# Optimization experiments

Measured on AMD Instinct MI355X. Metric: run time of the kernel, lower is better.

Reference implementation:

```python
import jax, jax.numpy as jnp
import numpy as np

LSTM_SIZE = 64
NUM_OPS = 5
NUM_LAYERS = 7  # 2 warmup anchors + 5 sampled layers (layer_id 2..6)


def _lstm_cell(x, h, c, w_ih, w_hh, b_ih, b_hh):
    # torch LSTMCell gate order: i, f, g, o
    g = x @ w_ih.T + b_ih + h @ w_hh.T + b_hh  # [1, 4*64]
    i, f, gg, o = jnp.split(g, 4, axis=1)
    c2 = jax.nn.sigmoid(f) * c + jax.nn.sigmoid(i) * jnp.tanh(gg)
    h2 = jax.nn.sigmoid(o) * jnp.tanh(c2)
    return h2, c2


def _sampler(embed, w_ih, w_hh, b_ih, b_hh, w_soft, b_soft, b_soft_no_learn,
             w_attn1, w_attn2, v_attn, prev_c, prev_h, use_bias, key):
    keys = jax.random.split(key, 20)  # 5 layers * (2 index + 2 op) samples
    k = 0
    anchors, anchors_w1, arc_seq = [], [], []
    log_prob = jnp.float32(0.0)
    entropy = jnp.float32(0.0)
    inputs = embed[0][None, :]
    # warmup: two anchor slots (anchors are zeros, per original code)
    for _ in range(2):
        prev_h, prev_c = _lstm_cell(inputs, prev_h, prev_c, w_ih, w_hh, b_ih, b_hh)
        anchors.append(jnp.zeros((1, LSTM_SIZE), jnp.float32))
        anchors_w1.append(prev_h @ w_attn1.T)
    for layer_id in range(2, NUM_LAYERS):
        idxs, ops = [], []
        # sample 2 previous-layer indices via tiny attention
        for _ in range(2):
            prev_h, prev_c = _lstm_cell(inputs, prev_h, prev_c, w_ih, w_hh, b_ih, b_hh)
            query = jnp.concatenate(anchors_w1, axis=0)            # [layer_id, 64]
            q = jnp.tanh(query + prev_h @ w_attn2.T)               # broadcast [layer_id, 64]
            logits = (q @ v_attn.T).reshape(layer_id)              # [layer_id]
            logits = logits / 5.0 + 1.1 * jnp.tanh(logits)
            index = jax.random.categorical(keys[k], logits); k += 1
            logp = jax.nn.log_softmax(logits)
            log_prob = log_prob + (-logp[index])
            entropy = entropy + jax.lax.stop_gradient(-jnp.sum(logp * jnp.exp(logp)))
            idxs.append(index)
            A = jnp.concatenate(anchors, axis=0)                   # [layer_id, 64]
            inputs = A[index][None, :]
        # sample 2 ops
        for _ in range(2):
            prev_h, prev_c = _lstm_cell(inputs, prev_h, prev_c, w_ih, w_hh, b_ih, b_hh)
            logits = (prev_h @ w_soft.T + b_soft)                  # [1, 5]
            logits = 1.1 / 2.5 * jnp.tanh(logits / 5.0)
            if use_bias:
                logits = logits + b_soft_no_learn
            logits = logits[0]
            op_id = jax.random.categorical(keys[k], logits); k += 1
            logp = jax.nn.log_softmax(logits)
            log_prob = log_prob + (-logp[op_id])
            entropy = entropy + jax.lax.stop_gradient(-jnp.sum(logp * jnp.exp(logp)))
            ops.append(op_id)
            inputs = embed[op_id + 1][None, :]
        # extra step producing this layer's anchor
        prev_h, prev_c = _lstm_cell(inputs, prev_h, prev_c, w_ih, w_hh, b_ih, b_hh)
        anchors.append(prev_h)
        anchors_w1.append(prev_h @ w_attn1.T)
        inputs = embed[0][None, :]
        # arc layout per layer after in-place fixups: [idx1, op1, idx2, op2]
        arc_seq += [idxs[0], ops[0], idxs[1], ops[1]]
    arc = jnp.stack(arc_seq)
    return arc, entropy, log_prob, prev_c, prev_h


def setup_inputs() -> dict:
    key = jax.random.key(0)
    ks = jax.random.split(key, 9)
    u = lambda k, shape: jax.random.uniform(k, shape, jnp.float32, -0.1, 0.1)
    return {
        "embed": u(ks[0], (6, LSTM_SIZE)),
        "w_ih": u(ks[1], (4 * LSTM_SIZE, LSTM_SIZE)),
        "w_hh": u(ks[2], (4 * LSTM_SIZE, LSTM_SIZE)),
        "b_ih": u(ks[3], (4 * LSTM_SIZE,)),
        "b_hh": u(ks[4], (4 * LSTM_SIZE,)),
        "w_soft": u(ks[5], (NUM_OPS, LSTM_SIZE)),
        "b_soft": jnp.array([[10.0, 10.0, 0.0, 0.0, 0.0]], jnp.float32),
        "b_soft_no_learn": jnp.array([[0.25, 0.25, -0.25, -0.25, -0.25]], jnp.float32),
        "w_attn1": u(ks[6], (LSTM_SIZE, LSTM_SIZE)),
        "w_attn2": u(ks[7], (LSTM_SIZE, LSTM_SIZE)),
        "v_attn": u(ks[8], (1, LSTM_SIZE)),
        "seed": 0,
    }


def reference(embed, w_ih, w_hh, b_ih, b_hh, w_soft, b_soft, b_soft_no_learn,
              w_attn1, w_attn2, v_attn, seed):
    key = jax.random.key(seed)
    k1, k2 = jax.random.split(key)
    zc = jnp.zeros((1, LSTM_SIZE), jnp.float32)
    zh = jnp.zeros((1, LSTM_SIZE), jnp.float32)
    arc1, ent1, lp1, c, h = _sampler(embed, w_ih, w_hh, b_ih, b_hh, w_soft, b_soft,
                                     b_soft_no_learn, w_attn1, w_attn2, v_attn,
                                     zc, zh, True, k1)
    arc2, ent2, lp2, _, _ = _sampler(embed, w_ih, w_hh, b_ih, b_hh, w_soft, b_soft,
                                     b_soft_no_learn, w_attn1, w_attn2, v_attn,
                                     c, h, False, k2)
    return (arc1, arc2, lp1 + lp2, ent1 + ent2)
```

## Files before the change

kernel.cpp:

```cpp
#include <hip/hip_runtime.h>
#include <cstdint>

#ifndef FASTMATH
#define FASTMATH 1
#endif

#define NT 512

__device__ __forceinline__ uint32_t rotl32_(uint32_t v, int d) {
  return (v << d) | (v >> (32 - d));
}

__device__ __forceinline__ void tf2x32(uint32_t k0, uint32_t k1,
                                       uint32_t x0, uint32_t x1,
                                       uint32_t& o0, uint32_t& o1) {
  const uint32_t k2 = k0 ^ k1 ^ 0x1BD11BDAu;
  x0 += k0; x1 += k1;
#define TF4(a,b,c,d) \
  x0 += x1; x1 = rotl32_(x1,a); x1 ^= x0; \
  x0 += x1; x1 = rotl32_(x1,b); x1 ^= x0; \
  x0 += x1; x1 = rotl32_(x1,c); x1 ^= x0; \
  x0 += x1; x1 = rotl32_(x1,d); x1 ^= x0;
  TF4(13,15,26,6)
  x0 += k1; x1 += k2 + 1u;
  TF4(17,29,16,24)
  x0 += k2; x1 += k0 + 2u;
  TF4(13,15,26,6)
  x0 += k0; x1 += k1 + 3u;
  TF4(17,29,16,24)
  x0 += k1; x1 += k2 + 4u;
  TF4(13,15,26,6)
  x0 += k2; x1 += k0 + 5u;
#undef TF4
  o0 = x0; o1 = x1;
}

#if FASTMATH
__device__ __forceinline__ float tanh_(float x) {
  float e = __expf(2.0f * x);
  return 1.0f - __fdividef(2.0f, e + 1.0f);
}
__device__ __forceinline__ float sig_(float x) {
  return __fdividef(1.0f, 1.0f + __expf(-x));
}
#define log_ __logf
#define exp_ __expf
#else
__device__ __forceinline__ float tanh_(float x) { return tanhf(x); }
__device__ __forceinline__ float sig_(float x) { return 0.5f * tanhf(0.5f * x) + 0.5f; }
#define log_ logf
#define exp_ expf
#endif

template <int CTRL>
__device__ __forceinline__ float dppf(float x) {
  return __int_as_float(__builtin_amdgcn_update_dpp(
      0, __float_as_int(x), CTRL, 0xF, 0xF, true));
}
template <int CTRL>
__device__ __forceinline__ int dppi(int x) {
  return __builtin_amdgcn_update_dpp(0, x, CTRL, 0xF, 0xF, true);
}
constexpr int QP1 = 0xB1;
constexpr int QP2 = 0x4E;
constexpr int HM  = 0x141;

__global__ __launch_bounds__(NT, 1)
void nas_controller(const float* __restrict__ embed,
                    const float* __restrict__ w_ih,
                    const float* __restrict__ w_hh,
                    const float* __restrict__ b_ih,
                    const float* __restrict__ b_hh,
                    const float* __restrict__ w_soft,
                    const float* __restrict__ b_soft,
                    const float* __restrict__ b_soft_nl,
                    const float* __restrict__ w_attn1,
                    const float* __restrict__ w_attn2,
                    const float* __restrict__ v_attn,
                    const int* __restrict__ seedp,
                    float* __restrict__ out) {
  const int tid  = threadIdx.x;
  const int lane = tid & 63;
  const int wid  = tid >> 6;
  const int row  = tid >> 1;
  const int half = tid & 1;

  __shared__ __align__(16) float attn1L[64 * 68];
  __shared__ __align__(16) float attn2L[64 * 68];
  __shared__ __align__(16) float wsoftL[5 * 68 + 8];
  __shared__ __align__(16) float vaL[64];
  __shared__ __align__(16) float preQ[13 * 256];
  __shared__ __align__(16) float aw1sL[8 * 68];
  __shared__ __align__(16) float hw2L[64];
  __shared__ __align__(16) float hB[64];
  __shared__ float gates[2][256];
  __shared__ float gL[320];
  __shared__ float lSave[320];
  __shared__ float lpT[40], entT[40];
  __shared__ int   biSave[40];
  __shared__ float bsoftL[8], bnlL[8];

  float4 wi[8], wh[8];
  {
    const float4* a = reinterpret_cast<const float4*>(w_ih) + row * 16 + half * 8;
#pragma unroll
    for (int j = 0; j < 8; ++j) wi[j] = a[j];
    const float4* b = reinterpret_cast<const float4*>(w_hh) + row * 16 + half * 8;
#pragma unroll
    for (int j = 0; j < 8; ++j) wh[j] = b[j];
  }
  const float bsi = b_ih[lane] + b_hh[lane];
  const float bsf = b_ih[64 + lane] + b_hh[64 + lane];
  const float bsg = b_ih[128 + lane] + b_hh[128 + lane];
  const float bso = b_ih[192 + lane] + b_hh[192 + lane];

  for (int i4 = tid; i4 < 1024; i4 += NT) {
    int r = i4 >> 4, c4 = i4 & 15;
    reinterpret_cast<float4*>(attn1L)[r * 17 + c4] =
        reinterpret_cast<const float4*>(w_attn1)[i4];
    reinterpret_cast<float4*>(attn2L)[r * 17 + c4] =
        reinterpret_cast<const float4*>(w_attn2)[i4];
  }
  for (int i = tid; i < 340; i += NT) {
    int r = i / 68, c = i % 68;
    wsoftL[i] = (c < 64) ? w_soft[r * 64 + c] : 0.f;
  }
  if (tid < 64) { vaL[tid] = v_attn[tid]; hB[tid] = 0.f; }
  if (tid < 256) gates[0][tid] = 0.f;
  if (tid < 8) {
    bsoftL[tid] = (tid < 5) ? b_soft[tid] : 0.f;
    bnlL[tid]   = (tid < 5) ? b_soft_nl[tid] : 0.f;
  }
  preQ[6 * 256 + tid] = 0.f;

  if (tid < 320) {
    int s_ = (tid >= 160) ? 1 : 0;
    int rem = tid - s_ * 160;
    int k = rem >> 3, i = rem & 7;
    uint32_t a, b, ka, kb, o0, o1;
    tf2x32(0u, (uint32_t)seedp[0], 0u, (uint32_t)s_, a, b);
    tf2x32(a, b, 0u, (uint32_t)k, ka, kb);
    tf2x32(ka, kb, 0u, (uint32_t)i, o0, o1);
    uint32_t bits = o0 ^ o1;
    const float TINY = 1.1754943508222875e-38f;
    float uu = __uint_as_float((bits >> 9) | 0x3f800000u) - 1.0f;
    uu = uu * (1.0f - TINY) + TINY;
    uu = fmaxf(TINY, uu);
    gL[tid] = -log_(-log_(uu));
  }

#pragma unroll
  for (int e = 0; e < 6; ++e) {
    const float4* x4 = reinterpret_cast<const float4*>(embed + e * 64) + half * 8;
    float a0 = 0, a1 = 0, a2 = 0, a3 = 0;
#pragma unroll
    for (int j = 0; j < 8; ++j) {
      float4 x = x4[j], w = wi[j];
      a0 = fmaf(w.x, x.x, a0); a1 = fmaf(w.y, x.y, a1);
      a2 = fmaf(w.z, x.z, a2); a3 = fmaf(w.w, x.w, a3);
    }
    float acc = (a0 + a1) + (a2 + a3);
    acc += __shfl_xor(acc, 1);
    if (half == 0) preQ[e * 256 + row] = acc;
  }

  __syncthreads();

  float creg = 0.f;
  int gp = 0, sIdx = 0;
  int srcSlot = 0;

  auto nonlinW0 = [&]() {
    const float* pq = preQ + srcSlot * 256;
    float gi = (gates[gp][lane]       + pq[lane])       + bsi;
    float gf = (gates[gp][64 + lane]  + pq[64 + lane])  + bsf;
    float gg = (gates[gp][128 + lane] + pq[128 + lane]) + bsg;
    float go = (gates[gp][192 + lane] + pq[192 + lane]) + bso;
    float c2 = sig_(gf) * creg + sig_(gi) * tanh_(gg);
    float h2 = sig_(go) * tanh_(c2);
    creg = c2;
    hB[lane] = h2;
  };

  auto hdotGW = [&]() {
    const float4* h4 = reinterpret_cast<const float4*>(hB) + half * 8;
    float a0 = 0, a1 = 0, a2 = 0, a3 = 0;
#pragma unroll
    for (int j = 0; j < 8; ++j) {
      float4 x = h4[j], w = wh[j];
      a0 = fmaf(w.x, x.x, a0); a1 = fmaf(w.y, x.y, a1);
      a2 = fmaf(w.z, x.z, a2); a3 = fmaf(w.w, x.w, a3);
    }
    float acc = (a0 + a1) + (a2 + a3);
    acc += __shfl_xor(acc, 1);
    if (half == 0) gates[gp ^ 1][row] = acc;
  };

  auto matvecAll = [&](const float* W, float* dst) {
    const int r8 = tid >> 3, q = tid & 7;
    const float4* w4 = reinterpret_cast<const float4*>(W + r8 * 68 + q * 8);
    float4 wa = w4[0], wb = w4[1];
    const float4* h4 = reinterpret_cast<const float4*>(hB) + q * 2;
    float4 ha = h4[0], hb = h4[1];
    float acc = fmaf(wa.x, ha.x, fmaf(wa.y, ha.y, fmaf(wa.z, ha.z, wa.w * ha.w)));
    acc += fmaf(wb.x, hb.x, fmaf(wb.y, hb.y, fmaf(wb.z, hb.z, wb.w * hb.w)));
    acc += __shfl_xor(acc, 1);
    acc += __shfl_xor(acc, 2);
    acc += __shfl_xor(acc, 4);
    if (q == 0) dst[r8] = acc;
  };

  auto anchorPre = [&](int slot) {
    const float4* h4 = reinterpret_cast<const float4*>(hB) + half * 8;
    float a0 = 0, a1 = 0, a2 = 0, a3 = 0;
#pragma unroll
    for (int j = 0; j < 8; ++j) {
      float4 x = h4[j], w = wi[j];
      a0 = fmaf(w.x, x.x, a0); a1 = fmaf(w.y, x.y, a1);
      a2 = fmaf(w.z, x.z, a2); a3 = fmaf(w.w, x.w, a3);
    }
    float acc = (a0 + a1) + (a2 + a3);
    acc += __shfl_xor(acc, 1);
    if (half == 0) preQ[slot * 256 + row] = acc;
  };

  auto argmaxSel = [&](int n, int k, float l, float* op) -> int {
    if (lane < 8) lSave[(sIdx * 20 + k) * 8 + lane] = l;
    float g = (lane < n) ? gL[sIdx * 160 + k * 8 + lane] : 0.f;
    float v = (lane < n) ? (l + g) : -INFINITY;
    int bi = lane & 7;
#define ARGSTEP(C) { float ov = dppf<C>(v); int oi = dppi<C>(bi); \
    bool tk = (ov > v) || (ov == v && oi < bi); if (tk) { v = ov; bi = oi; } }
    ARGSTEP(QP1) ARGSTEP(QP2) ARGSTEP(HM)
#undef ARGSTEP
    if (lane == 0) {
      biSave[sIdx * 20 + k] = bi;
      op[0] = (float)bi;
    }
    return __builtin_amdgcn_readfirstlane(bi);
  };

  auto idxSel = [&](int n, int k, float* op) -> int {
    const int g8 = lane >> 3, j = lane & 7;
    float sacc = 0.f;
    if (g8 < n) {
      const float4* aw = reinterpret_cast<const float4*>(aw1sL + g8 * 68 + j * 8);
      const float4* hq = reinterpret_cast<const float4*>(hw2L + j * 8);
      const float4* vq = reinterpret_cast<const float4*>(vaL + j * 8);
      float4 A0 = aw[0], A1 = aw[1], H0 = hq[0], H1 = hq[1], V0 = vq[0], V1 = vq[1];
      sacc = fmaf(tanh_(A0.x + H0.x), V0.x, sacc);
      sacc = fmaf(tanh_(A0.y + H0.y), V0.y, sacc);
      sacc = fmaf(tanh_(A0.z + H0.z), V0.z, sacc);
      sacc = fmaf(tanh_(A0.w + H0.w), V0.w, sacc);
      sacc = fmaf(tanh_(A1.x + H1.x), V1.x, sacc);
      sacc = fmaf(tanh_(A1.y + H1.y), V1.y, sacc);
      sacc = fmaf(tanh_(A1.z + H1.z), V1.z, sacc);
      sacc = fmaf(tanh_(A1.w + H1.w), V1.w, sacc);
    }
    sacc += dppf<QP1>(sacc); sacc += dppf<QP2>(sacc); sacc += dppf<HM>(sacc);
    float raw = __shfl(sacc, lane << 3);
    float l = (lane < n) ? (raw / 5.0f + 1.1f * tanh_(raw)) : -INFINITY;
    return argmaxSel(n, k, l, op);
  };

  auto opSel = [&](int k, int mode, float* op) -> int {
    const int g8 = lane >> 3, j = lane & 7;
    float sacc = 0.f;
    if (g8 < 5) {
      const float4* wq = reinterpret_cast<const float4*>(wsoftL + g8 * 68 + j * 8);
      float4 wa = wq[0], wb = wq[1];
      const float4* h4 = reinterpret_cast<const float4*>(hB) + j * 2;
      float4 ha = h4[0], hb = h4[1];
      sacc = fmaf(wa.x, ha.x, fmaf(wa.y, ha.y, fmaf(wa.z, ha.z, wa.w * ha.w)));
      sacc += fmaf(wb.x, hb.x, fmaf(wb.y, hb.y, fmaf(wb.z, hb.z, wb.w * hb.w)));
    }
    sacc += dppf<QP1>(sacc); sacc += dppf<QP2>(sacc); sacc += dppf<HM>(sacc);
    float raw = __shfl(sacc, lane << 3) + bsoftL[lane & 7];
    float l;
    if (lane < 5) {
      l = (float)(1.1 / 2.5) * tanh_(raw / 5.0f);
      if (mode == 1) l += bnlL[lane];
    } else l = -INFINITY;
    return argmaxSel(5, k, l, op);
  };

  for (int s = 0; s < 2; ++s) {
    sIdx = s;
    const int opMode = (s == 0) ? 1 : 2;
    for (int w = 0; w < 2; ++w) {
      if (wid == 0) nonlinW0();
      __syncthreads();
      matvecAll(attn1L, aw1sL + w * 68);
      hdotGW();
      __syncthreads(); gp ^= 1;
    }
    int keyk = 0;
    for (int L = 2; L <= 6; ++L) {
      float* ob = out + s * 20 + (L - 2) * 4;
      if (wid == 0) nonlinW0();
      __syncthreads();
      matvecAll(attn2L, hw2L);
      hdotGW();
      __syncthreads(); gp ^= 1;
      if (wid == 0) {
        srcSlot = 6 + idxSel(L, keyk, ob + 0);
        nonlinW0();
      }
      keyk++;
      __syncthreads();
      matvecAll(attn2L, hw2L);
      hdotGW();
      __syncthreads(); gp ^= 1;
      if (wid == 0) {
        srcSlot = 6 + idxSel(L, keyk, ob + 2);
        nonlinW0();
        srcSlot = 1 + opSel(keyk + 1, opMode, ob + 1);
      }
      keyk += 2;
      __syncthreads();
      hdotGW();
      __syncthreads(); gp ^= 1;
      if (wid == 0) {
        nonlinW0();
        srcSlot = 1 + opSel(keyk, opMode, ob + 3);
      }
      keyk++;
      __syncthreads();
      hdotGW();
      __syncthreads(); gp ^= 1;
      if (wid == 0) {
        nonlinW0();
        srcSlot = 0;
      }
      __syncthreads();
      matvecAll(attn1L, aw1sL + L * 68);
      anchorPre(6 + L);
      hdotGW();
      __syncthreads(); gp ^= 1;
    }
  }

  if (tid < 320) {
    int j = tid >> 3, c = tid & 7;
    float l = lSave[j * 8 + c];
    float mx = l;
    mx = fmaxf(mx, dppf<QP1>(mx)); mx = fmaxf(mx, dppf<QP2>(mx)); mx = fmaxf(mx, dppf<HM>(mx));
    float e = (l == -INFINITY) ? 0.f : exp_(l - mx);
    float ss = e; ss += dppf<QP1>(ss); ss += dppf<QP2>(ss); ss += dppf<HM>(ss);
    float lse = log_(ss);
    float lpi = l - mx - lse;
    float ec = (l == -INFINITY) ? 0.f : lpi * exp_(lpi);
    ec += dppf<QP1>(ec); ec += dppf<QP2>(ec); ec += dppf<HM>(ec);
    if (c == 0) entT[j] = -ec;
    if (c == biSave[j]) lpT[j] = -(l - mx - lse);
  }
  __syncthreads();
  if (tid == 0) {
    float lp = 0.f, ent = 0.f;
    for (int j = 0; j < 40; ++j) { lp += lpT[j]; ent += entT[j]; }
    out[40] = lp; out[41] = ent;
  }
}

extern "C" void kernel_launch(void* const* d_in, const int* in_sizes, int n_in,
                              void* d_out, int out_size, void* d_ws, size_t ws_size,
                              hipStream_t stream) {
  (void)in_sizes; (void)n_in; (void)out_size; (void)d_ws; (void)ws_size;
  nas_controller<<<1, NT, 0, stream>>>(
      (const float*)d_in[0],
      (const float*)d_in[1],
      (const float*)d_in[2],
      (const float*)d_in[3],
      (const float*)d_in[4],
      (const float*)d_in[5],
      (const float*)d_in[6],
      (const float*)d_in[7],
      (const float*)d_in[8],
      (const float*)d_in[9],
      (const float*)d_in[10],
      (const int*)d_in[11],
      (float*)d_out);
}
```

Measured before the change: 69.70 us.

## Interleave gate preactivations as float4 and prefetch candidate input rows

Gate and precomputed input-projection buffers are stored interleaved per unit, with the i,f,g,o values of one unit next to each other, so the serial wave-0 nonlinearity reads one float4 per buffer instead of four scalar LDS loads. The next step's input projection is prefetched into registers. For attention-selected inputs, all six candidate rows are loaded before the sampling result is known and then chosen with selects, taking the LDS load off the path that waits on the sample. This costs extra registers and extra speculative LDS reads.

```diff
diff --git a/kernel.cpp b/kernel.cpp
--- a/kernel.cpp
+++ b/kernel.cpp
@@ -84,21 +84,25 @@
   const int wid  = tid >> 6;
   const int row  = tid >> 1;
   const int half = tid & 1;
+  const int ru   = row & 63;
+  const int rg   = row >> 6;
 
   __shared__ __align__(16) float attn1L[64 * 68];
   __shared__ __align__(16) float attn2L[64 * 68];
   __shared__ __align__(16) float wsoftL[5 * 68 + 8];
   __shared__ __align__(16) float vaL[64];
-  __shared__ __align__(16) float preQ[13 * 256];
+  __shared__ __align__(16) float4 preQ4[13 * 64];
+  __shared__ __align__(16) float4 gates4[2][64];
   __shared__ __align__(16) float aw1sL[8 * 68];
   __shared__ __align__(16) float hw2L[64];
   __shared__ __align__(16) float hB[64];
-  __shared__ float gates[2][256];
   __shared__ float gL[320];
   __shared__ float lSave[320];
   __shared__ float lpT[40], entT[40];
   __shared__ int   biSave[40];
   __shared__ float bsoftL[8], bnlL[8];
+
+  float* preQf  = reinterpret_cast<float*>(preQ4);
 
   float4 wi[8], wh[8];
   {
@@ -126,12 +130,12 @@
     wsoftL[i] = (c < 64) ? w_soft[r * 64 + c] : 0.f;
   }
   if (tid < 64) { vaL[tid] = v_attn[tid]; hB[tid] = 0.f; }
-  if (tid < 256) gates[0][tid] = 0.f;
+  if (tid < 64) gates4[0][tid] = make_float4(0.f, 0.f, 0.f, 0.f);
   if (tid < 8) {
     bsoftL[tid] = (tid < 5) ? b_soft[tid] : 0.f;
     bnlL[tid]   = (tid < 5) ? b_soft_nl[tid] : 0.f;
   }
-  preQ[6 * 256 + tid] = 0.f;
+  preQf[6 * 256 + tid] = 0.f;
 
   if (tid < 320) {
     int s_ = (tid >= 160) ? 1 : 0;
@@ -161,21 +165,21 @@
     }
     float acc = (a0 + a1) + (a2 + a3);
     acc += __shfl_xor(acc, 1);
-    if (half == 0) preQ[e * 256 + row] = acc;
+    if (half == 0) preQf[(e * 64 + ru) * 4 + rg] = acc;
   }
 
   __syncthreads();
 
   float creg = 0.f;
   int gp = 0, sIdx = 0;
-  int srcSlot = 0;
-
-  auto nonlinW0 = [&]() {
-    const float* pq = preQ + srcSlot * 256;
-    float gi = (gates[gp][lane]       + pq[lane])       + bsi;
-    float gf = (gates[gp][64 + lane]  + pq[64 + lane])  + bsf;
-    float gg = (gates[gp][128 + lane] + pq[128 + lane]) + bsg;
-    float go = (gates[gp][192 + lane] + pq[192 + lane]) + bso;
+  float4 p4next;
+  if (wid == 0) p4next = preQ4[lane];
+
+  auto nonlinW0 = [&](const float4& g4, const float4& p4) {
+    float gi = (g4.x + p4.x) + bsi;
+    float gf = (g4.y + p4.y) + bsf;
+    float gg = (g4.z + p4.z) + bsg;
+    float go = (g4.w + p4.w) + bso;
     float c2 = sig_(gf) * creg + sig_(gi) * tanh_(gg);
     float h2 = sig_(go) * tanh_(c2);
     creg = c2;
@@ -193,7 +197,8 @@
     }
     float acc = (a0 + a1) + (a2 + a3);
     acc += __shfl_xor(acc, 1);
-    if (half == 0) gates[gp ^ 1][row] = acc;
+    if (half == 0)
+      reinterpret_cast<float*>(&gates4[gp ^ 1][0])[ru * 4 + rg] = acc;
   };
 
   auto matvecAll = [&](const float* W, float* dst) {
@@ -221,7 +226,7 @@
     }
     float acc = (a0 + a1) + (a2 + a3);
     acc += __shfl_xor(acc, 1);
-    if (half == 0) preQ[slot * 256 + row] = acc;
+    if (half == 0) preQf[(slot * 64 + ru) * 4 + rg] = acc;
   };
 
   auto argmaxSel = [&](int n, int k, float l, float* op) -> int {
@@ -284,11 +289,23 @@
     return argmaxSel(5, k, l, op);
   };
 
+  auto sel6 = [&](int sel, const float4& c0, const float4& c1, const float4& c2,
+                  const float4& c3, const float4& c4, const float4& c5) -> float4 {
+    float4 a01 = (sel == 1) ? c1 : c0;
+    float4 a23 = (sel == 3) ? c3 : c2;
+    float4 a45 = (sel == 5) ? c5 : c4;
+    return (sel < 2) ? a01 : ((sel < 4) ? a23 : a45);
+  };
+
   for (int s = 0; s < 2; ++s) {
     sIdx = s;
     const int opMode = (s == 0) ? 1 : 2;
     for (int w = 0; w < 2; ++w) {
-      if (wid == 0) nonlinW0();
+      if (wid == 0) {
+        float4 g4 = gates4[gp][lane];
+        nonlinW0(g4, p4next);
+        p4next = preQ4[lane];
+      }
       __syncthreads();
       matvecAll(attn1L, aw1sL + w * 68);
       hdotGW();
@@ -297,14 +314,21 @@
     int keyk = 0;
     for (int L = 2; L <= 6; ++L) {
       float* ob = out + s * 20 + (L - 2) * 4;
-      if (wid == 0) nonlinW0();
+      if (wid == 0) {
+        float4 g4 = gates4[gp][lane];
+        nonlinW0(g4, p4next);
+      }
       __syncthreads();
       matvecAll(attn2L, hw2L);
       hdotGW();
       __syncthreads(); gp ^= 1;
       if (wid == 0) {
-        srcSlot = 6 + idxSel(L, keyk, ob + 0);
-        nonlinW0();
+        float4 c0 = preQ4[6 * 64 + lane],  c1 = preQ4[7 * 64 + lane];
+        float4 c2 = preQ4[8 * 64 + lane],  c3 = preQ4[9 * 64 + lane];
+        float4 c4 = preQ4[10 * 64 + lane], c5 = preQ4[11 * 64 + lane];
+        float4 g4 = gates4[gp][lane];
+        int sel = idxSel(L, keyk, ob + 0);
+        nonlinW0(g4, sel6(sel, c0, c1, c2, c3, c4, c5));
       }
       keyk++;
       __syncthreads();
@@ -312,25 +336,33 @@
       hdotGW();
       __syncthreads(); gp ^= 1;
       if (wid == 0) {
-        srcSlot = 6 + idxSel(L, keyk, ob + 2);
-        nonlinW0();
-        srcSlot = 1 + opSel(keyk + 1, opMode, ob + 1);
+        float4 c0 = preQ4[6 * 64 + lane],  c1 = preQ4[7 * 64 + lane];
+        float4 c2 = preQ4[8 * 64 + lane],  c3 = preQ4[9 * 64 + lane];
+        float4 c4 = preQ4[10 * 64 + lane], c5 = preQ4[11 * 64 + lane];
+        float4 g4 = gates4[gp][lane];
+        int sel = idxSel(L, keyk, ob + 2);
+        nonlinW0(g4, sel6(sel, c0, c1, c2, c3, c4, c5));
+        int sel2 = opSel(keyk + 1, opMode, ob + 1);
+        p4next = preQ4[(1 + sel2) * 64 + lane];
       }
       keyk += 2;
       __syncthreads();
       hdotGW();
       __syncthreads(); gp ^= 1;
       if (wid == 0) {
-        nonlinW0();
-        srcSlot = 1 + opSel(keyk, opMode, ob + 3);
+        float4 g4 = gates4[gp][lane];
+        nonlinW0(g4, p4next);
+        int sel = opSel(keyk, opMode, ob + 3);
+        p4next = preQ4[(1 + sel) * 64 + lane];
       }
       keyk++;
       __syncthreads();
       hdotGW();
       __syncthreads(); gp ^= 1;
       if (wid == 0) {
-        nonlinW0();
-        srcSlot = 0;
+        float4 g4 = gates4[gp][lane];
+        nonlinW0(g4, p4next);
+        p4next = preQ4[lane];
       }
       __syncthreads();
       matvecAll(attn1L, aw1sL + L * 68);
```

Measured after the change: 70.10 us. No clear change (+0.6%).
